# Performance work log

Hardware: AMD Instinct MI355X
Metric: run time of the kernel (lower is better)

Reference implementation:

```python
import jax, jax.numpy as jnp
import numpy as np

B, C, H, W = 8, 256, 64, 64
GROUPS = 32
EPS = 1e-6


def setup_inputs() -> dict:
    key = jax.random.key(0)
    ks = jax.random.split(key, 8)
    s = 0.02
    return {
        "x": jax.random.normal(ks[0], (B, C, H, W), dtype=jnp.float32),
        "gn_scale": jnp.ones((C,), jnp.float32),
        "gn_bias": jnp.zeros((C,), jnp.float32),
        "wq": jax.random.normal(ks[1], (C, C), jnp.float32) * s,
        "bq": jnp.zeros((C,), jnp.float32),
        "wk": jax.random.normal(ks[2], (C, C), jnp.float32) * s,
        "bk": jnp.zeros((C,), jnp.float32),
        "wv": jax.random.normal(ks[3], (C, C), jnp.float32) * s,
        "bv": jnp.zeros((C,), jnp.float32),
        "wproj": jax.random.normal(ks[4], (C, C), jnp.float32) * s,
        "bproj": jnp.zeros((C,), jnp.float32),
    }


def _group_norm(x, scale, bias):
    b, c, h, w = x.shape
    xg = x.reshape(b, GROUPS, c // GROUPS, h, w)
    mean = xg.mean(axis=(2, 3, 4), keepdims=True)
    var = xg.var(axis=(2, 3, 4), keepdims=True)
    xn = ((xg - mean) * jax.lax.rsqrt(var + EPS)).reshape(b, c, h, w)
    return xn * scale[None, :, None, None] + bias[None, :, None, None]


def _conv1x1(x, w, b):
    # 1x1 conv == channel-mixing matmul: w is [out_ch, in_ch]
    return jnp.einsum("oc,bchw->bohw", w, x) + b[None, :, None, None]


def reference(x, gn_scale, gn_bias, wq, bq, wk, bk, wv, bv, wproj, bproj):
    b, c, h, w = x.shape
    hn = _group_norm(x, gn_scale, gn_bias)
    q = _conv1x1(hn, wq, bq).reshape(b, c, h * w)  # [b,c,n]
    k = _conv1x1(hn, wk, bk).reshape(b, c, h * w)
    v = _conv1x1(hn, wv, bv).reshape(b, c, h * w)
    # scores[b,n,m] = <q[:, :, n], k[:, :, m]> * c^-0.5  (softmax over keys m)
    scale = jnp.asarray(c, x.dtype) ** -0.5
    attn = jax.nn.softmax(jnp.einsum("bcn,bcm->bnm", q, k) * scale, axis=2)
    # h_[b,c,n] = sum_m v[b,c,m] * attn[b,n,m]
    h_ = jnp.einsum("bcm,bnm->bcn", v, attn).reshape(b, c, h, w)
    h_ = _conv1x1(h_, wproj, bproj)
    return x + h_
```

## Files before the change

### kernel.cpp

```cpp
#include <hip/hip_runtime.h>

#define B_ 8
#define C_ 256
#define N_ 4096
#define G_ 32

typedef __bf16 bf16;
typedef __bf16 bf16x8 __attribute__((ext_vector_type(8)));
typedef float f32x4 __attribute__((ext_vector_type(4)));
typedef long i64;
typedef long i64x2 __attribute__((ext_vector_type(2)));
typedef unsigned int u32;
typedef unsigned char u8;
typedef unsigned short u16;
typedef unsigned short __attribute__((may_alias)) u16a;
typedef long __attribute__((may_alias)) i64a;

__device__ __forceinline__ f32x4 mfma16(bf16x8 a, bf16x8 b, f32x4 c) {
    return __builtin_amdgcn_mfma_f32_16x16x32_bf16(a, b, c, 0, 0, 0);
}
__device__ __forceinline__ f32x4 mfma_fp8(i64 a, i64 b, f32x4 c) {
    return __builtin_amdgcn_mfma_f32_16x16x32_fp8_fp8(a, b, c, 0, 0, 0);
}

typedef __attribute__((address_space(1))) const void* gas_t;
typedef __attribute__((address_space(3))) void* las_t;
__device__ __forceinline__ void gl2lds16(const void* g, void* l) {
    __builtin_amdgcn_global_load_lds((gas_t)g, (las_t)l, 16, 0, 0);
}

__device__ __forceinline__ u32 f32_to_fp8(float x) {
    union { float f; u32 u; } c;
    c.f = x;
    u32 s = (c.u >> 24) & 0x80;
    u32 m = (c.u & 0x7fffffff) + 0x00080000;
    int e = (int)(m >> 23) - 127;
    if (e < -6) return s;
    if (e > 8) return s | 0x7e;
    u32 v = ((u32)(e + 7) << 3) | ((m >> 20) & 7);
    if (v > 0x7e) v = 0x7e;
    return s | v;
}
__device__ __forceinline__ u32 fp8_fast(float x) {
    union { float f; u32 u; } c;
    c.f = x;
    return ((c.u + 0x00080000u) >> 20) - 960u;
}

__global__ __launch_bounds__(256) void gn_stats(const float* __restrict__ x,
                                                float* __restrict__ gstats) {
    int blk = blockIdx.x;
    int b = blk >> 5, g = blk & 31;
    int tid = threadIdx.x;
    int c = g * 8 + (tid >> 5);
    const float* row = x + ((size_t)(b * C_ + c)) * N_;
    float s = 0.f, s2 = 0.f;
    for (int n = (tid & 31) * 4; n < N_; n += 128) {
        float4 v = *(const float4*)(row + n);
        s += v.x + v.y + v.z + v.w;
        s2 += v.x * v.x + v.y * v.y + v.z * v.z + v.w * v.w;
    }
    for (int off = 32; off; off >>= 1) {
        s += __shfl_xor(s, off);
        s2 += __shfl_xor(s2, off);
    }
    __shared__ float red[8];
    int wid = tid >> 6;
    if ((tid & 63) == 0) { red[wid] = s; red[4 + wid] = s2; }
    __syncthreads();
    if (tid == 0) {
        float S = red[0] + red[1] + red[2] + red[3];
        float S2 = red[4] + red[5] + red[6] + red[7];
        float mean = S * (1.f / 32768.f);
        float var = S2 * (1.f / 32768.f) - mean * mean;
        gstats[blk * 2] = mean;
        gstats[blk * 2 + 1] = rsqrtf(var + 1e-6f);
    }
}

__global__ __launch_bounds__(256) void gn_apply(const float* __restrict__ x,
                                                const float* __restrict__ gsc,
                                                const float* __restrict__ gbi,
                                                const float* __restrict__ gstats,
                                                bf16* __restrict__ hn) {
    __shared__ float tile[32][33];
    int b = blockIdx.z, c0 = blockIdx.y * 32, n0 = blockIdx.x * 32;
    int tx = threadIdx.x & 31, ty = threadIdx.x >> 5;
    for (int i = 0; i < 4; i++) {
        int cl = ty + i * 8;
        int c = c0 + cl;
        int g = c >> 3;
        float mean = gstats[(b * G_ + g) * 2];
        float rstd = gstats[(b * G_ + g) * 2 + 1];
        float sc = gsc[c] * rstd;
        float bs = gbi[c] - mean * sc;
        float v = x[((size_t)(b * C_ + c)) * N_ + n0 + tx];
        tile[cl][tx] = v * sc + bs;
    }
    __syncthreads();
    for (int i = 0; i < 4; i++) {
        int nl = ty + i * 8;
        hn[((size_t)(b * N_ + n0 + nl)) * C_ + c0 + tx] = (bf16)tile[tx][nl];
    }
}

__global__ __launch_bounds__(256) void cvt_w(const float* __restrict__ wq,
                                             const float* __restrict__ wk,
                                             const float* __restrict__ wv,
                                             const float* __restrict__ wp,
                                             bf16* __restrict__ dst) {
    int i = blockIdx.x * 256 + threadIdx.x;
    dst[i] = (bf16)wq[i];
    dst[65536 + i] = (bf16)wk[i];
    dst[131072 + i] = (bf16)wv[i];
    dst[196608 + i] = (bf16)wp[i];
}

__global__ __launch_bounds__(256) void gemm_qkv(const bf16* __restrict__ A,
                                                const bf16* __restrict__ Wq,
                                                const bf16* __restrict__ Wk,
                                                const bf16* __restrict__ Wv,
                                                const float* __restrict__ bq,
                                                const float* __restrict__ bk,
                                                const float* __restrict__ bv,
                                                u8* __restrict__ q8,
                                                u8* __restrict__ k8,
                                                u8* __restrict__ v8) {
    __shared__ __align__(16) bf16 As[64][32];
    __shared__ __align__(16) bf16 Wqs[64][32];
    __shared__ __align__(16) bf16 Wks[64][32];
    __shared__ __align__(16) bf16 Wvs[64][32];
    int m0 = blockIdx.x * 64;
    int n0 = blockIdx.y * 64;
    int tid = threadIdx.x;
    int wv_ = tid >> 6, lane = tid & 63, lr = lane & 15, lq = lane >> 4;
    int wm = (wv_ & 1) * 32, wn = (wv_ >> 1) * 32;
    int sr = tid >> 2, sk = (tid & 3) * 8;
    f32x4 qacc[2][2] = {}, kacc[2][2] = {}, vacc[2][2] = {};
    for (int kk = 0; kk < C_; kk += 32) {
        __syncthreads();
        gl2lds16(&A[(size_t)(m0 + sr) * C_ + kk + sk], &As[sr][sk]);
        gl2lds16(&Wq[(size_t)(n0 + sr) * C_ + kk + sk], &Wqs[sr][sk]);
        gl2lds16(&Wk[(size_t)(n0 + sr) * C_ + kk + sk], &Wks[sr][sk]);
        gl2lds16(&Wv[(size_t)(n0 + sr) * C_ + kk + sk], &Wvs[sr][sk]);
        __syncthreads();
        bf16x8 a0 = *(const bf16x8*)&As[wm + lr][lq * 8];
        bf16x8 a1 = *(const bf16x8*)&As[wm + 16 + lr][lq * 8];
        bf16x8 q0 = *(const bf16x8*)&Wqs[wn + lr][lq * 8];
        bf16x8 q1 = *(const bf16x8*)&Wqs[wn + 16 + lr][lq * 8];
        bf16x8 k0 = *(const bf16x8*)&Wks[wn + lr][lq * 8];
        bf16x8 k1 = *(const bf16x8*)&Wks[wn + 16 + lr][lq * 8];
        bf16x8 v0 = *(const bf16x8*)&Wvs[wn + lr][lq * 8];
        bf16x8 v1 = *(const bf16x8*)&Wvs[wn + 16 + lr][lq * 8];
        qacc[0][0] = mfma16(a0, q0, qacc[0][0]);
        qacc[0][1] = mfma16(a0, q1, qacc[0][1]);
        qacc[1][0] = mfma16(a1, q0, qacc[1][0]);
        qacc[1][1] = mfma16(a1, q1, qacc[1][1]);
        kacc[0][0] = mfma16(a0, k0, kacc[0][0]);
        kacc[0][1] = mfma16(a0, k1, kacc[0][1]);
        kacc[1][0] = mfma16(a1, k0, kacc[1][0]);
        kacc[1][1] = mfma16(a1, k1, kacc[1][1]);
        vacc[0][0] = mfma16(a0, v0, vacc[0][0]);
        vacc[0][1] = mfma16(a0, v1, vacc[0][1]);
        vacc[1][0] = mfma16(a1, v0, vacc[1][0]);
        vacc[1][1] = mfma16(a1, v1, vacc[1][1]);
    }
    for (int i = 0; i < 2; i++)
        for (int j = 0; j < 2; j++) {
            int col = n0 + wn + j * 16 + lr;
            int p = (col & 0xC0) | ((col & 0x18) << 1) | ((col & 0x20) >> 2) | (col & 7);
            float bvq = bq[col], bvk = bk[col], bvv = bv[col];
            for (int r = 0; r < 4; r++) {
                int row = m0 + wm + i * 16 + lq * 4 + r;
                q8[(size_t)row * C_ + p] = (u8)f32_to_fp8(qacc[i][j][r] + bvq);
                k8[(size_t)row * C_ + p] = (u8)f32_to_fp8(kacc[i][j][r] + bvk);
                int bb = row >> 12, n = row & (N_ - 1);
                v8[((size_t)(bb * C_ + col)) * N_ + (n & ~31) +
                   (((n & 15) << 1) | ((n >> 4) & 1))] =
                    (u8)f32_to_fp8(vacc[i][j][r] + bvv);
            }
        }
}

__global__ __launch_bounds__(128, 2) void attn(const u8* __restrict__ q,
                                               const u8* __restrict__ k,
                                               const u8* __restrict__ vT,
                                               bf16* __restrict__ O0,
                                               bf16* __restrict__ O1,
                                               float* __restrict__ lp) {
    __shared__ __align__(16) u8 smem[35840];
    u8* Ks = smem;
    u8* Vt = smem + 16384;
    u8* Ps = smem + 32768;

    int b = blockIdx.z, h = blockIdx.y, q0 = blockIdx.x * 64;
    int tid = threadIdx.x;
    int w = tid >> 6, lane = tid & 63, lr = lane & 15, lq = lane >> 4;

    const u8* kglob = k + ((size_t)(b * N_) + h * 2048) * 256;
    const u8* vglob = vT + (size_t)b * C_ * N_ + h * 2048;

    u32 offK[4], offV[4];
#pragma unroll
    for (int j = 0; j < 4; j++) {
        int p = ((w * 4 + j) << 6) + lane;
        int rK = p >> 4, cK = (p & 15) ^ (rK & 15);
        offK[j] = rK * 256 + cK * 16;
        int rV = p >> 1, cV = (p & 1) ^ ((rV >> 2) & 1);
        offV[j] = rV * N_ + cV * 16;
    }

    i64x2 qf[2][4];
#pragma unroll
    for (int t = 0; t < 2; t++) {
        const u8* qrow = q + ((size_t)(b * N_ + q0 + w * 32 + t * 16 + lr)) * 256;
#pragma unroll
        for (int tq = 0; tq < 4; tq++)
            qf[t][tq] = *(const i64x2*)&qrow[tq * 64 + lq * 16];
    }

    f32x4 oacc[2][16] = {};
    float li[2][4] = {};
    u8* Pw = Ps + w * 1536;

#pragma unroll
    for (int j = 0; j < 4; j++) {
        gl2lds16(kglob + offK[j], Ks + ((w * 4 + j) << 10));
        gl2lds16(vglob + offV[j], Vt + ((w * 4 + j) << 10));
    }

    for (int mt = 0; mt < 64; mt++) {
        int cur = mt & 1;
        __syncthreads();

        if (mt < 63) {
            const u8* kit = kglob + (size_t)(mt + 1) * 32 * 256;
            const u8* vit = vglob + (mt + 1) * 32;
#pragma unroll
            for (int j = 0; j < 4; j++) {
                gl2lds16(kit + offK[j], Ks + (cur ^ 1) * 8192 + ((w * 4 + j) << 10));
                gl2lds16(vit + offV[j], Vt + (cur ^ 1) * 8192 + ((w * 4 + j) << 10));
            }
        }

        const u8* Kb = Ks + cur * 8192;
        const u8* Vb = Vt + cur * 8192;

        f32x4 st[2][2] = {};
#pragma unroll
        for (int kt = 0; kt < 2; kt++) {
            int r = kt * 16 + lr;
#pragma unroll
            for (int tq = 0; tq < 4; tq++) {
                i64x2 kf = *(const i64x2*)&Kb[r * 256 + (((tq * 4 + lq) ^ (r & 15)) << 4)];
                st[0][kt] = mfma_fp8(qf[0][tq].x, kf.x, st[0][kt]);
                st[0][kt] = mfma_fp8(qf[0][tq].y, kf.y, st[0][kt]);
                st[1][kt] = mfma_fp8(qf[1][tq].x, kf.x, st[1][kt]);
                st[1][kt] = mfma_fp8(qf[1][tq].y, kf.y, st[1][kt]);
            }
        }

#pragma unroll
        for (int t = 0; t < 2; t++)
#pragma unroll
            for (int r = 0; r < 4; r++) {
                float e0 = __expf(st[t][0][r] * 0.0625f);
                float e1 = __expf(st[t][1][r] * 0.0625f);
                li[t][r] += e0 + e1;
                u16 pk = (u16)((fp8_fast(e0) & 0xff) | ((fp8_fast(e1) & 0xff) << 8));
                *(u16a*)&Pw[(t * 16 + lq * 4 + r) * 48 + lr * 2] = pk;
            }

        __threadfence_block();

        i64 pf[2];
#pragma unroll
        for (int t = 0; t < 2; t++)
            pf[t] = *(const i64a*)&Pw[(t * 16 + lr) * 48 + lq * 8];
#pragma unroll
        for (int ct = 0; ct < 16; ct++) {
            int row = ct * 16 + lr;
            i64 vf = *(const i64a*)&Vb[row * 32 + (((lq >> 1) ^ ((row >> 2) & 1)) << 4) +
                                       ((lq & 1) << 3)];
            oacc[0][ct] = mfma_fp8(pf[0], vf, oacc[0][ct]);
            oacc[1][ct] = mfma_fp8(pf[1], vf, oacc[1][ct]);
        }
    }

    float lsum[2][4];
#pragma unroll
    for (int t = 0; t < 2; t++)
#pragma unroll
        for (int r = 0; r < 4; r++) {
            float s = li[t][r];
            s += __shfl_xor(s, 1);
            s += __shfl_xor(s, 2);
            s += __shfl_xor(s, 4);
            s += __shfl_xor(s, 8);
            lsum[t][r] = s;
        }

    bf16* Op = h ? O1 : O0;
#pragma unroll
    for (int t = 0; t < 2; t++)
#pragma unroll
        for (int ct = 0; ct < 16; ct++)
#pragma unroll
            for (int r = 0; r < 4; r++)
                Op[((size_t)(b * N_ + q0 + w * 32 + t * 16 + lq * 4 + r)) * C_ + ct * 16 + lr] =
                    (bf16)oacc[t][ct][r];
    if (lr == 0) {
        float* lrow = lp + ((size_t)(h * B_ + b)) * N_ + q0 + w * 32;
#pragma unroll
        for (int t = 0; t < 2; t++)
#pragma unroll
            for (int r = 0; r < 4; r++) lrow[t * 16 + lq * 4 + r] = lsum[t][r];
    }
}

__global__ __launch_bounds__(256) void proj_res(const bf16* __restrict__ W,
                                                const bf16* __restrict__ O0,
                                                const bf16* __restrict__ O1,
                                                const float* __restrict__ lp,
                                                const float* __restrict__ bias,
                                                const float* __restrict__ x,
                                                float* __restrict__ out) {
    __shared__ __align__(16) bf16 Ws[64][32];
    __shared__ __align__(16) bf16 As[64][32];
    int m0 = blockIdx.x * 64;
    int n0 = blockIdx.y * 64;
    int tid = threadIdx.x;
    int wv_ = tid >> 6, lane = tid & 63, lr = lane & 15, lq = lane >> 4;
    int wm = (wv_ & 1) * 32, wn = (wv_ >> 1) * 32;
    int sr = tid >> 2, sk = (tid & 3) * 8;
    int T = n0 + sr, bb = T >> 12, nn = T & (N_ - 1);
    float inv = 1.f / (lp[(size_t)bb * N_ + nn] + lp[(size_t)(B_ + bb) * N_ + nn]);
    f32x4 acc[2][2] = {};
    for (int kk = 0; kk < C_; kk += 32) {
        __syncthreads();
        gl2lds16(&W[(size_t)(m0 + sr) * C_ + kk + sk], &Ws[sr][sk]);
        bf16x8 o0 = *(const bf16x8*)&O0[(size_t)T * C_ + kk + sk];
        bf16x8 o1 = *(const bf16x8*)&O1[(size_t)T * C_ + kk + sk];
        bf16x8 cm;
#pragma unroll
        for (int e = 0; e < 8; e++) cm[e] = (bf16)(((float)o0[e] + (float)o1[e]) * inv);
        *(bf16x8*)&As[sr][sk] = cm;
        __syncthreads();
        bf16x8 a0 = *(const bf16x8*)&Ws[wm + lr][lq * 8];
        bf16x8 a1 = *(const bf16x8*)&Ws[wm + 16 + lr][lq * 8];
        bf16x8 b0 = *(const bf16x8*)&As[wn + lr][lq * 8];
        bf16x8 b1 = *(const bf16x8*)&As[wn + 16 + lr][lq * 8];
        acc[0][0] = mfma16(a0, b0, acc[0][0]);
        acc[0][1] = mfma16(a0, b1, acc[0][1]);
        acc[1][0] = mfma16(a1, b0, acc[1][0]);
        acc[1][1] = mfma16(a1, b1, acc[1][1]);
    }
    for (int i = 0; i < 2; i++)
        for (int j = 0; j < 2; j++) {
            int Tt = n0 + wn + j * 16 + lr;
            int b = Tt >> 12, n = Tt & (N_ - 1);
            for (int r = 0; r < 4; r++) {
                int o = m0 + wm + i * 16 + lq * 4 + r;
                size_t idx = ((size_t)(b * C_ + o)) * N_ + n;
                out[idx] = x[idx] + acc[i][j][r] + bias[o];
            }
        }
}

extern "C" void kernel_launch(void* const* d_in, const int* in_sizes, int n_in,
                              void* d_out, int out_size, void* d_ws, size_t ws_size,
                              hipStream_t stream) {
    const float* x = (const float*)d_in[0];
    const float* gsc = (const float*)d_in[1];
    const float* gbi = (const float*)d_in[2];
    const float* wq = (const float*)d_in[3];
    const float* bq = (const float*)d_in[4];
    const float* wk = (const float*)d_in[5];
    const float* bk = (const float*)d_in[6];
    const float* wv = (const float*)d_in[7];
    const float* bv = (const float*)d_in[8];
    const float* wp = (const float*)d_in[9];
    const float* bp = (const float*)d_in[10];
    float* out = (float*)d_out;

    const size_t SZ = (size_t)B_ * N_ * C_;
    char* ws = (char*)d_ws;
    float* gstats = (float*)ws;
    bf16* wb = (bf16*)(ws + 4096);
    char* base = ws + 4096 + 524288;
    bf16* hn = (bf16*)base;
    u8* q8 = (u8*)(base + SZ * 2);
    u8* k8 = (u8*)(base + SZ * 3);
    u8* v8 = (u8*)(base + SZ * 4);
    bf16* O0 = (bf16*)base;
    bf16* O1 = (bf16*)(base + SZ * 5);
    float* lpart = (float*)(base + SZ * 7);

    cvt_w<<<256, 256, 0, stream>>>(wq, wk, wv, wp, wb);
    gn_stats<<<B_ * G_, 256, 0, stream>>>(x, gstats);
    gn_apply<<<dim3(N_ / 32, C_ / 32, B_), 256, 0, stream>>>(x, gsc, gbi, gstats, hn);
    gemm_qkv<<<dim3(B_ * N_ / 64, C_ / 64), 256, 0, stream>>>(
        hn, wb, wb + 65536, wb + 131072, bq, bk, bv, q8, k8, v8);
    attn<<<dim3(N_ / 64, 2, B_), 128, 0, stream>>>(q8, k8, v8, O0, O1, lpart);
    proj_res<<<dim3(C_ / 64, B_ * N_ / 64), 256, 0, stream>>>(
        wb + 196608, O0, O1, lpart, bp, x, out);
}
```

Baseline: 307.5 us.

## Keep softmax probabilities in registers via transposed QK MFMA and remap blocks

Swaps the A/B operands of the QK^T fp8 MFMA so each lane's score accumulators already match the operand layout the PV MFMA needs. The probabilities can then be packed into fp8 registers directly, which drops the per-wave LDS scratch, the fence and the LDS reload. The V permutation written by the QKV kernel and the row-sum reduction lanes are changed to match. Blocks are also remapped so consecutive workgroups are spread across batch and half indices, which changes locality and XCD distribution. The V layout change must agree exactly with the new register mapping.

```diff
diff --git a/kernel.cpp b/kernel.cpp
--- a/kernel.cpp
+++ b/kernel.cpp
@@ -13,7 +13,7 @@
 typedef unsigned int u32;
 typedef unsigned char u8;
 typedef unsigned short u16;
-typedef unsigned short __attribute__((may_alias)) u16a;
+typedef unsigned long long u64;
 typedef long __attribute__((may_alias)) i64a;
 
 __device__ __forceinline__ f32x4 mfma16(bf16x8 a, bf16x8 b, f32x4 c) {
@@ -175,8 +175,9 @@
                 q8[(size_t)row * C_ + p] = (u8)f32_to_fp8(qacc[i][j][r] + bvq);
                 k8[(size_t)row * C_ + p] = (u8)f32_to_fp8(kacc[i][j][r] + bvk);
                 int bb = row >> 12, n = row & (N_ - 1);
+                int n5 = n & 31;
                 v8[((size_t)(bb * C_ + col)) * N_ + (n & ~31) +
-                   (((n & 15) << 1) | ((n >> 4) & 1))] =
+                   (((n5 & 12) << 1) | ((n5 & 16) >> 2) | (n5 & 3))] =
                     (u8)f32_to_fp8(vacc[i][j][r] + bvv);
             }
         }
@@ -188,12 +189,15 @@
                                                bf16* __restrict__ O0,
                                                bf16* __restrict__ O1,
                                                float* __restrict__ lp) {
-    __shared__ __align__(16) u8 smem[35840];
+    __shared__ __align__(16) u8 smem[32768];
     u8* Ks = smem;
     u8* Vt = smem + 16384;
-    u8* Ps = smem + 32768;
-
-    int b = blockIdx.z, h = blockIdx.y, q0 = blockIdx.x * 64;
+
+    int flat = blockIdx.x + (blockIdx.y << 6) + (blockIdx.z << 7);
+    int nid = (flat & 7) * 128 + (flat >> 3);
+    int q0 = (nid & 63) * 64;
+    int h = (nid >> 6) & 1;
+    int b = nid >> 7;
     int tid = threadIdx.x;
     int w = tid >> 6, lane = tid & 63, lr = lane & 15, lq = lane >> 4;
 
@@ -220,8 +224,7 @@
     }
 
     f32x4 oacc[2][16] = {};
-    float li[2][4] = {};
-    u8* Pw = Ps + w * 1536;
+    float li[2] = {};
 
 #pragma unroll
     for (int j = 0; j < 4; j++) {
@@ -253,30 +256,31 @@
 #pragma unroll
             for (int tq = 0; tq < 4; tq++) {
                 i64x2 kf = *(const i64x2*)&Kb[r * 256 + (((tq * 4 + lq) ^ (r & 15)) << 4)];
-                st[0][kt] = mfma_fp8(qf[0][tq].x, kf.x, st[0][kt]);
-                st[0][kt] = mfma_fp8(qf[0][tq].y, kf.y, st[0][kt]);
-                st[1][kt] = mfma_fp8(qf[1][tq].x, kf.x, st[1][kt]);
-                st[1][kt] = mfma_fp8(qf[1][tq].y, kf.y, st[1][kt]);
+                st[0][kt] = mfma_fp8(kf.x, qf[0][tq].x, st[0][kt]);
+                st[0][kt] = mfma_fp8(kf.y, qf[0][tq].y, st[0][kt]);
+                st[1][kt] = mfma_fp8(kf.x, qf[1][tq].x, st[1][kt]);
+                st[1][kt] = mfma_fp8(kf.y, qf[1][tq].y, st[1][kt]);
             }
         }
 
-#pragma unroll
-        for (int t = 0; t < 2; t++)
-#pragma unroll
-            for (int r = 0; r < 4; r++) {
-                float e0 = __expf(st[t][0][r] * 0.0625f);
-                float e1 = __expf(st[t][1][r] * 0.0625f);
-                li[t][r] += e0 + e1;
-                u16 pk = (u16)((fp8_fast(e0) & 0xff) | ((fp8_fast(e1) & 0xff) << 8));
-                *(u16a*)&Pw[(t * 16 + lq * 4 + r) * 48 + lr * 2] = pk;
-            }
-
-        __threadfence_block();
-
         i64 pf[2];
 #pragma unroll
-        for (int t = 0; t < 2; t++)
-            pf[t] = *(const i64a*)&Pw[(t * 16 + lr) * 48 + lq * 8];
+        for (int qt = 0; qt < 2; qt++) {
+            float e[2][4];
+#pragma unroll
+            for (int kt = 0; kt < 2; kt++)
+#pragma unroll
+                for (int r = 0; r < 4; r++)
+                    e[kt][r] = __expf(st[qt][kt][r] * 0.0625f);
+            li[qt] += ((e[0][0] + e[0][1]) + (e[0][2] + e[0][3])) +
+                      ((e[1][0] + e[1][1]) + (e[1][2] + e[1][3]));
+            u32 lo = (fp8_fast(e[0][0]) & 0xff) | ((fp8_fast(e[0][1]) & 0xff) << 8) |
+                     ((fp8_fast(e[0][2]) & 0xff) << 16) | (fp8_fast(e[0][3]) << 24);
+            u32 hi = (fp8_fast(e[1][0]) & 0xff) | ((fp8_fast(e[1][1]) & 0xff) << 8) |
+                     ((fp8_fast(e[1][2]) & 0xff) << 16) | (fp8_fast(e[1][3]) << 24);
+            pf[qt] = (i64)(((u64)hi << 32) | lo);
+        }
+
 #pragma unroll
         for (int ct = 0; ct < 16; ct++) {
             int row = ct * 16 + lr;
@@ -287,18 +291,14 @@
         }
     }
 
-    float lsum[2][4];
-#pragma unroll
-    for (int t = 0; t < 2; t++)
-#pragma unroll
-        for (int r = 0; r < 4; r++) {
-            float s = li[t][r];
-            s += __shfl_xor(s, 1);
-            s += __shfl_xor(s, 2);
-            s += __shfl_xor(s, 4);
-            s += __shfl_xor(s, 8);
-            lsum[t][r] = s;
-        }
+    float lsum[2];
+#pragma unroll
+    for (int qt = 0; qt < 2; qt++) {
+        float s = li[qt];
+        s += __shfl_xor(s, 16);
+        s += __shfl_xor(s, 32);
+        lsum[qt] = s;
+    }
 
     bf16* Op = h ? O1 : O0;
 #pragma unroll
@@ -309,12 +309,10 @@
             for (int r = 0; r < 4; r++)
                 Op[((size_t)(b * N_ + q0 + w * 32 + t * 16 + lq * 4 + r)) * C_ + ct * 16 + lr] =
                     (bf16)oacc[t][ct][r];
-    if (lr == 0) {
+    if (lq == 0) {
         float* lrow = lp + ((size_t)(h * B_ + b)) * N_ + q0 + w * 32;
 #pragma unroll
-        for (int t = 0; t < 2; t++)
-#pragma unroll
-            for (int r = 0; r < 4; r++) lrow[t * 16 + lq * 4 + r] = lsum[t][r];
+        for (int qt = 0; qt < 2; qt++) lrow[qt * 16 + lr] = lsum[qt];
     }
 }
 
```

Measured after the change: 306.6 us. About the same (-0.3%).
